# Kernel optimization log

Hardware: AMD Instinct MI355X
Metric: run time of the kernel (lower is better)

## Reference

```python
import jax, jax.numpy as jnp
import numpy as np

N_FEATURES = 256
SEQ_LEN = 128
N_HIDDEN = 30
N_LAYERS = 2
BATCH = 1024


def _lstm_layer(x, w_ih, w_hh, b_ih, b_hh):
    # x: [B, T, I]; w_ih: [4H, I]; w_hh: [4H, H]; biases: [4H]
    # PyTorch gate order: i, f, g, o
    B = x.shape[0]
    H = w_hh.shape[1]
    # precompute input contribution for all timesteps: [B, T, 4H]
    xg = jnp.einsum('bti,gi->btg', x, w_ih) + (b_ih + b_hh)
    xg = jnp.swapaxes(xg, 0, 1)  # [T, B, 4H]

    def step(carry, xg_t):
        h, c = carry
        gates = xg_t + h @ w_hh.T  # [B, 4H]
        i, f, g, o = jnp.split(gates, 4, axis=-1)
        i = jax.nn.sigmoid(i)
        f = jax.nn.sigmoid(f)
        g = jnp.tanh(g)
        o = jax.nn.sigmoid(o)
        c = f * c + i * g
        h = o * jnp.tanh(c)
        return (h, c), h

    h0 = jnp.zeros((B, H), dtype=x.dtype)
    c0 = jnp.zeros((B, H), dtype=x.dtype)
    _, hs = jax.lax.scan(step, (h0, c0), xg)
    return jnp.swapaxes(hs, 0, 1)  # [B, T, H]


def setup_inputs() -> dict:
    key = jax.random.key(0)
    ks = jax.random.split(key, 12)
    s_in = 1.0 / np.sqrt(N_HIDDEN)
    G = 4 * N_HIDDEN
    inp = {
        'x': jax.random.normal(ks[0], (BATCH, SEQ_LEN, N_FEATURES), dtype=jnp.float32),
        'w_ih0': jax.random.uniform(ks[1], (G, N_FEATURES), jnp.float32, -s_in, s_in),
        'w_hh0': jax.random.uniform(ks[2], (G, N_HIDDEN), jnp.float32, -s_in, s_in),
        'b_ih0': jax.random.uniform(ks[3], (G,), jnp.float32, -s_in, s_in),
        'b_hh0': jax.random.uniform(ks[4], (G,), jnp.float32, -s_in, s_in),
        'w_ih1': jax.random.uniform(ks[5], (G, N_HIDDEN), jnp.float32, -s_in, s_in),
        'w_hh1': jax.random.uniform(ks[6], (G, N_HIDDEN), jnp.float32, -s_in, s_in),
        'b_ih1': jax.random.uniform(ks[7], (G,), jnp.float32, -s_in, s_in),
        'b_hh1': jax.random.uniform(ks[8], (G,), jnp.float32, -s_in, s_in),
        'w_lin': jax.random.uniform(ks[9], (1, N_HIDDEN * SEQ_LEN), jnp.float32, -s_in, s_in),
        'b_lin': jax.random.uniform(ks[10], (1,), jnp.float32, -s_in, s_in),
    }
    return inp


def reference(x, w_ih0, w_hh0, b_ih0, b_hh0, w_ih1, w_hh1, b_ih1, b_hh1, w_lin, b_lin):
    h1 = _lstm_layer(x, w_ih0, w_hh0, b_ih0, b_hh0)   # [B, T, H]
    h2 = _lstm_layer(h1, w_ih1, w_hh1, b_ih1, b_hh1)  # [B, T, H]
    flat = h2.reshape(h2.shape[0], -1)                 # [B, T*H]
    return flat @ w_lin.T + b_lin                      # [B, 1]
```

## Files before the change

### kernel.cpp

```cpp
#include <hip/hip_runtime.h>

#define T_SEQ 128
#define NF 256
#define NH 30
#define NG 120
#define NBATCH 1024
#define M_ROWS (NBATCH * T_SEQ)

#define BIAS_OFF 0
#define BHI_OFF  1024
#define BLO_OFF  (BHI_OFF + 65536)
#define XG_OFF_B (BLO_OFF + 65536)

typedef __attribute__((ext_vector_type(8))) short short8;
typedef __attribute__((ext_vector_type(2))) float float2v;
typedef __attribute__((ext_vector_type(4))) float float4v;

__device__ __forceinline__ short bf16_of(float f) {
  union { float f; unsigned u; } v; v.f = f;
  unsigned r = v.u + 0x7fffu + ((v.u >> 16) & 1u);
  return (short)(r >> 16);
}
__device__ __forceinline__ float f_of_bf16(short s) {
  union { unsigned u; float f; } v; v.u = ((unsigned)(unsigned short)s) << 16;
  return v.f;
}

__device__ __forceinline__ float fast_rcp(float x) { return __builtin_amdgcn_rcpf(x); }

#define L2E 1.4426950408889634f
__device__ __forceinline__ float sigm_fast(float x) {
  float e = __builtin_amdgcn_exp2f(-L2E * x);
  return fast_rcp(1.0f + e);
}
__device__ __forceinline__ float act_a(float x, float kIn_l2, float kOut, float cOut) {
  float e = __builtin_amdgcn_exp2f(-kIn_l2 * x);
  return fmaf(kOut, fast_rcp(1.0f + e), cOut);
}
__device__ __forceinline__ float tanh_fast(float x) {
  float e = __builtin_amdgcn_exp2f(-2.0f * L2E * x);
  return fmaf(2.0f, fast_rcp(1.0f + e), -1.0f);
}

__device__ __forceinline__ float2v fma2(float2v a, float2v b, float2v c) {
  return __builtin_elementwise_fma(a, b, c);
}

__global__ void prep_kernel(const float* __restrict__ w_ih0,
                            const float* __restrict__ b_ih0,
                            const float* __restrict__ b_hh0,
                            unsigned char* __restrict__ ws) {
  int gid = blockIdx.x * 256 + threadIdx.x;
  float* bias = (float*)(ws + BIAS_OFF);
  if (gid < 128) {
    int og = (gid & 3) * NH + (gid >> 2);
    bias[gid] = (gid < NG) ? (b_ih0[og] + b_hh0[og]) : 0.0f;
  }

  int lane = gid & 63;
  int ts = gid >> 6;
  int t = ts >> 3, s = ts & 7;
  int n = s * 16 + (lane & 15);
  int orig = (n & 3) * NH + (n >> 2);
  int k0 = t * 32 + (lane >> 4) * 8;

  short8 hi, lo;
#pragma unroll
  for (int j = 0; j < 8; ++j) {
    float v = (n < NG) ? w_ih0[orig * NF + k0 + j] : 0.0f;
    short h = bf16_of(v);
    hi[j] = h;
    lo[j] = bf16_of(v - f_of_bf16(h));
  }
  *(short8*)(ws + BHI_OFF + (size_t)gid * 16) = hi;
  *(short8*)(ws + BLO_OFF + (size_t)gid * 16) = lo;
}

__global__ __launch_bounds__(256, 3) void gemm_xg(const float* __restrict__ x,
                                                  const unsigned char* __restrict__ ws,
                                                  float* __restrict__ xg) {
  __shared__ short lds_B[2][8 * 2 * 64 * 8];
  const int tid = threadIdx.x;
  const int lane = tid & 63;
  const int wave = tid >> 6;
  const int r15 = lane & 15;
  const int quad = lane >> 4;
  const int rowbase = blockIdx.x * 128 + wave * 32;

  const short* __restrict__ Bhi = (const short*)(ws + BHI_OFF);
  const short* __restrict__ Blo = (const short*)(ws + BLO_OFF);
  const float* __restrict__ bias = (const float*)(ws + BIAS_OFF);

  float4v acc[2][8];
#pragma unroll
  for (int s = 0; s < 8; ++s) {
    float b = bias[s * 16 + r15];
    float4v bv = {b, b, b, b};
    acc[0][s] = bv;
    acc[1][s] = bv;
  }

  const float* xptr[2];
  xptr[0] = x + (size_t)(rowbase + r15) * NF + quad * 8;
  xptr[1] = x + (size_t)(rowbase + 16 + r15) * NF + quad * 8;

#pragma unroll
  for (int i = 0; i < 2; ++i) {
    int s = wave * 2 + i;
    const short* ghi = Bhi + ((size_t)(0 * 8 + s) * 64 + lane) * 8;
    const short* glo = Blo + ((size_t)(0 * 8 + s) * 64 + lane) * 8;
    short* lhi = &lds_B[0][(s * 2 + 0) * 64 * 8];
    short* llo = &lds_B[0][(s * 2 + 1) * 64 * 8];
    __builtin_amdgcn_global_load_lds((const __attribute__((address_space(1))) void*)ghi,
                                     (__attribute__((address_space(3))) void*)lhi, 16, 0, 0);
    __builtin_amdgcn_global_load_lds((const __attribute__((address_space(1))) void*)glo,
                                     (__attribute__((address_space(3))) void*)llo, 16, 0, 0);
  }

  short8 ahi[2], alo[2];
#pragma unroll
  for (int g = 0; g < 2; ++g) {
    float4 p0 = *(const float4*)(xptr[g] + 0);
    float4 p1 = *(const float4*)(xptr[g] + 4);
    float f[8] = {p0.x, p0.y, p0.z, p0.w, p1.x, p1.y, p1.z, p1.w};
#pragma unroll
    for (int j = 0; j < 8; ++j) {
      short h = bf16_of(f[j]);
      ahi[g][j] = h;
      alo[g][j] = bf16_of(f[j] - f_of_bf16(h));
    }
  }
  __syncthreads();

  for (int t = 0; t < 8; ++t) {
    const int buf = t & 1;
    float4 anx[2][2];
    if (t < 7) {
#pragma unroll
      for (int i = 0; i < 2; ++i) {
        int s = wave * 2 + i;
        const short* ghi = Bhi + ((size_t)((t + 1) * 8 + s) * 64 + lane) * 8;
        const short* glo = Blo + ((size_t)((t + 1) * 8 + s) * 64 + lane) * 8;
        short* lhi = &lds_B[buf ^ 1][(s * 2 + 0) * 64 * 8];
        short* llo = &lds_B[buf ^ 1][(s * 2 + 1) * 64 * 8];
        __builtin_amdgcn_global_load_lds((const __attribute__((address_space(1))) void*)ghi,
                                         (__attribute__((address_space(3))) void*)lhi, 16, 0, 0);
        __builtin_amdgcn_global_load_lds((const __attribute__((address_space(1))) void*)glo,
                                         (__attribute__((address_space(3))) void*)llo, 16, 0, 0);
      }
#pragma unroll
      for (int g = 0; g < 2; ++g) {
        anx[g][0] = *(const float4*)(xptr[g] + (t + 1) * 32);
        anx[g][1] = *(const float4*)(xptr[g] + (t + 1) * 32 + 4);
      }
    }

#pragma unroll
    for (int s = 0; s < 8; ++s) {
      const short8 bh = *(const short8*)&lds_B[buf][((s * 2 + 0) * 64 + lane) * 8];
      const short8 bl = *(const short8*)&lds_B[buf][((s * 2 + 1) * 64 + lane) * 8];
#pragma unroll
      for (int g = 0; g < 2; ++g) {
        acc[g][s] = __builtin_amdgcn_mfma_f32_16x16x32_bf16(ahi[g], bh, acc[g][s], 0, 0, 0);
        acc[g][s] = __builtin_amdgcn_mfma_f32_16x16x32_bf16(ahi[g], bl, acc[g][s], 0, 0, 0);
        acc[g][s] = __builtin_amdgcn_mfma_f32_16x16x32_bf16(alo[g], bh, acc[g][s], 0, 0, 0);
      }
    }

    if (t < 7) {
#pragma unroll
      for (int g = 0; g < 2; ++g) {
        float f[8] = {anx[g][0].x, anx[g][0].y, anx[g][0].z, anx[g][0].w,
                      anx[g][1].x, anx[g][1].y, anx[g][1].z, anx[g][1].w};
#pragma unroll
        for (int j = 0; j < 8; ++j) {
          short h = bf16_of(f[j]);
          ahi[g][j] = h;
          alo[g][j] = bf16_of(f[j] - f_of_bf16(h));
        }
      }
    }
    __syncthreads();
  }

#pragma unroll
  for (int g = 0; g < 2; ++g) {
    const int row0 = rowbase + g * 16 + quad * 4;
#pragma unroll
    for (int s = 0; s < 8; ++s) {
      const int col = s * 16 + r15;
      if (col < NG) {
#pragma unroll
        for (int i = 0; i < 4; ++i) {
          xg[(size_t)(row0 + i) * NG + col] = acc[g][s][i];
        }
      }
    }
  }
}

__global__ __launch_bounds__(64, 1) void lstm_fused(const float* __restrict__ xg,
                                                    const float* __restrict__ w_hh0,
                                                    const float* __restrict__ w_ih1,
                                                    const float* __restrict__ w_hh1,
                                                    const float* __restrict__ b_ih1,
                                                    const float* __restrict__ b_hh1,
                                                    const float* __restrict__ w_lin,
                                                    const float* __restrict__ b_lin,
                                                    float* __restrict__ out) {
  __shared__ __align__(16) float hbuf0[32];
  __shared__ __align__(16) float hbuf1[32];
  const int b = blockIdx.x;
  const int lane = threadIdx.x;
  const bool hiHalf = lane >= 32;
  const int l = hiHalf ? (lane - 32) : lane;
  const int lc = (l < NH) ? l : (NH - 1);
  const int gA = hiHalf ? (60 + lc) : lc;
  const int gB = gA + NH;

  const float kInA = (hiHalf ? 2.0f : 1.0f) * L2E;
  const float kOutA = hiHalf ? 2.0f : 1.0f;
  const float cOutA = hiHalf ? -1.0f : 0.0f;

  float2v W0A[15], W0B[15], V1A[15], V1B[15], U1A[15], U1B[15];
#pragma unroll
  for (int p = 0; p < 15; ++p) {
    W0A[p] = *(const float2v*)&w_hh0[gA * NH + 2 * p];
    W0B[p] = *(const float2v*)&w_hh0[gB * NH + 2 * p];
    V1A[p] = *(const float2v*)&w_ih1[gA * NH + 2 * p];
    V1B[p] = *(const float2v*)&w_ih1[gB * NH + 2 * p];
    U1A[p] = *(const float2v*)&w_hh1[gA * NH + 2 * p];
    U1B[p] = *(const float2v*)&w_hh1[gB * NH + 2 * p];
  }
  const float bA1 = b_ih1[gA] + b_hh1[gA];
  const float bB1 = b_ih1[gB] + b_hh1[gB];

  float4v h0q[8], h1q[8];
#pragma unroll
  for (int k = 0; k < 8; ++k) {
    h0q[k] = float4v{0.f, 0.f, 0.f, 0.f};
    h1q[k] = float4v{0.f, 0.f, 0.f, 0.f};
  }

  float c0 = 0.0f, c1 = 0.0f, acc = 0.0f;
  const float* __restrict__ xgb = xg + (size_t)b * T_SEQ * NG;
  const int xoff = 4 * lc + (hiHalf ? 2 : 0);

  float2v xab[4];
  float wlr[4];
#pragma unroll
  for (int p = 0; p < 3; ++p) {
    xab[p] = *(const float2v*)&xgb[p * NG + xoff];
    wlr[p] = w_lin[p * NH + lc];
  }

#pragma unroll 4
  for (int t = 0; t < T_SEQ; ++t) {
    const int cur = t & 3;
    const int nxt = (t + 3) & 3;
    const int tp = (t + 3 < T_SEQ) ? (t + 3) : (T_SEQ - 1);
    float2v pxg = *(const float2v*)&xgb[tp * NG + xoff];
    float pwl = w_lin[tp * NH + lc];

    float2v a0A = {xab[cur].x, 0.f};
    float2v a0B = {xab[cur].y, 0.f};
#pragma unroll
    for (int k = 0; k < 8; ++k) {
      float2v hlo = __builtin_shufflevector(h0q[k], h0q[k], 0, 1);
      a0A = fma2(hlo, W0A[2 * k], a0A);
      a0B = fma2(hlo, W0B[2 * k], a0B);
      if (k < 7) {
        float2v hhi = __builtin_shufflevector(h0q[k], h0q[k], 2, 3);
        a0A = fma2(hhi, W0A[2 * k + 1], a0A);
        a0B = fma2(hhi, W0B[2 * k + 1], a0B);
      }
    }
    float sA = a0A.x + a0A.y;
    float sB = a0B.x + a0B.y;
    float aA = act_a(sA, kInA, kOutA, cOutA);
    float aB = sigm_fast(sB);
    float gg = __shfl_down(aA, 32);
    float oo = __shfl_down(aB, 32);
    c0 = fmaf(aB, c0, aA * gg);
    float h0 = oo * tanh_fast(c0);
    if (lane < NH) hbuf0[lane] = h0;
#pragma unroll
    for (int k = 0; k < 8; ++k) h0q[k] = *(const float4v*)&hbuf0[4 * k];

    float2v aUA = {bA1, 0.f};
    float2v aUB = {bB1, 0.f};
#pragma unroll
    for (int k = 0; k < 8; ++k) {
      float2v hlo = __builtin_shufflevector(h1q[k], h1q[k], 0, 1);
      aUA = fma2(hlo, U1A[2 * k], aUA);
      aUB = fma2(hlo, U1B[2 * k], aUB);
      if (k < 7) {
        float2v hhi = __builtin_shufflevector(h1q[k], h1q[k], 2, 3);
        aUA = fma2(hhi, U1A[2 * k + 1], aUA);
        aUB = fma2(hhi, U1B[2 * k + 1], aUB);
      }
    }

    float2v aVA = {0.f, 0.f};
    float2v aVB = {0.f, 0.f};
#pragma unroll
    for (int k = 0; k < 8; ++k) {
      float2v hlo = __builtin_shufflevector(h0q[k], h0q[k], 0, 1);
      aVA = fma2(hlo, V1A[2 * k], aVA);
      aVB = fma2(hlo, V1B[2 * k], aVB);
      if (k < 7) {
        float2v hhi = __builtin_shufflevector(h0q[k], h0q[k], 2, 3);
        aVA = fma2(hhi, V1A[2 * k + 1], aVA);
        aVB = fma2(hhi, V1B[2 * k + 1], aVB);
      }
    }
    float s1A = (aUA.x + aUA.y) + (aVA.x + aVA.y);
    float s1B = (aUB.x + aUB.y) + (aVB.x + aVB.y);
    float a1A = act_a(s1A, kInA, kOutA, cOutA);
    float a1B = sigm_fast(s1B);
    float gg1 = __shfl_down(a1A, 32);
    float oo1 = __shfl_down(a1B, 32);
    c1 = fmaf(a1B, c1, a1A * gg1);
    float h1 = oo1 * tanh_fast(c1);
    if (lane < NH) hbuf1[lane] = h1;
#pragma unroll
    for (int k = 0; k < 8; ++k) h1q[k] = *(const float4v*)&hbuf1[4 * k];

    acc = fmaf(h1, wlr[cur], acc);

    xab[nxt] = pxg;
    wlr[nxt] = pwl;
  }

  if (lane >= NH) acc = 0.0f;
#pragma unroll
  for (int off = 32; off > 0; off >>= 1) acc += __shfl_xor(acc, off);
  if (lane == 0) out[b] = acc + b_lin[0];
}

extern "C" void kernel_launch(void* const* d_in, const int* in_sizes, int n_in,
                              void* d_out, int out_size, void* d_ws, size_t ws_size,
                              hipStream_t stream) {
  (void)in_sizes; (void)n_in; (void)out_size; (void)ws_size;
  const float* x     = (const float*)d_in[0];
  const float* w_ih0 = (const float*)d_in[1];
  const float* w_hh0 = (const float*)d_in[2];
  const float* b_ih0 = (const float*)d_in[3];
  const float* b_hh0 = (const float*)d_in[4];
  const float* w_ih1 = (const float*)d_in[5];
  const float* w_hh1 = (const float*)d_in[6];
  const float* b_ih1 = (const float*)d_in[7];
  const float* b_hh1 = (const float*)d_in[8];
  const float* w_lin = (const float*)d_in[9];
  const float* b_lin = (const float*)d_in[10];
  unsigned char* ws = (unsigned char*)d_ws;
  float* out = (float*)d_out;
  float* xg = (float*)(ws + XG_OFF_B);

  prep_kernel<<<16, 256, 0, stream>>>(w_ih0, b_ih0, b_hh0, ws);
  gemm_xg<<<M_ROWS / 128, 256, 0, stream>>>(x, ws, xg);
  lstm_fused<<<NBATCH, 64, 0, stream>>>(xg, w_hh0, w_ih1, w_hh1,
                                        b_ih1, b_hh1, w_lin, b_lin, out);
}
```

Measured before the change: 302.3 us.

## Pipeline LSTM layers across two waves per batch with LDS staging

Splits the fused two-layer recurrence into a producer wave (layer 0 plus part of the layer-1 input projection) and a consumer wave (layer-1 recurrence), with four batch rows per 512-thread block. The waves hand off through double-buffered LDS and block barriers, so layer 0 of step t overlaps layer 1 of step t-1. Hidden-state broadcast now uses readlane instead of an LDS round trip. The cost is a block-wide barrier every step that couples the four batch rows in the block, plus higher register use from the scalar weight arrays.

```diff
diff --git a/kernel.cpp b/kernel.cpp
--- a/kernel.cpp
+++ b/kernel.cpp
@@ -6,6 +6,7 @@
 #define NG 120
 #define NBATCH 1024
 #define M_ROWS (NBATCH * T_SEQ)
+#define BPB 4
 
 #define BIAS_OFF 0
 #define BHI_OFF  1024
@@ -13,7 +14,6 @@
 #define XG_OFF_B (BLO_OFF + 65536)
 
 typedef __attribute__((ext_vector_type(8))) short short8;
-typedef __attribute__((ext_vector_type(2))) float float2v;
 typedef __attribute__((ext_vector_type(4))) float float4v;
 
 __device__ __forceinline__ short bf16_of(float f) {
@@ -26,6 +26,9 @@
   return v.f;
 }
 
+__device__ __forceinline__ float rl(float v, int j) {
+  return __int_as_float(__builtin_amdgcn_readlane(__float_as_int(v), j));
+}
 __device__ __forceinline__ float fast_rcp(float x) { return __builtin_amdgcn_rcpf(x); }
 
 #define L2E 1.4426950408889634f
@@ -42,9 +45,7 @@
   return fmaf(2.0f, fast_rcp(1.0f + e), -1.0f);
 }
 
-__device__ __forceinline__ float2v fma2(float2v a, float2v b, float2v c) {
-  return __builtin_elementwise_fma(a, b, c);
-}
+#define PIPE_BARRIER() asm volatile("s_waitcnt lgkmcnt(0)\n\ts_barrier" ::: "memory")
 
 __global__ void prep_kernel(const float* __restrict__ w_ih0,
                             const float* __restrict__ b_ih0,
@@ -199,7 +200,7 @@
   }
 }
 
-__global__ __launch_bounds__(64, 1) void lstm_fused(const float* __restrict__ xg,
+__global__ __launch_bounds__(512, 2) void lstm_pipe(const float* __restrict__ xg,
                                                     const float* __restrict__ w_hh0,
                                                     const float* __restrict__ w_ih1,
                                                     const float* __restrict__ w_hh1,
@@ -208,10 +209,16 @@
                                                     const float* __restrict__ w_lin,
                                                     const float* __restrict__ b_lin,
                                                     float* __restrict__ out) {
-  __shared__ __align__(16) float hbuf0[32];
-  __shared__ __align__(16) float hbuf1[32];
-  const int b = blockIdx.x;
-  const int lane = threadIdx.x;
+  __shared__ __align__(16) float stage[BPB][2][48];
+  __shared__ __align__(16) float vstage[BPB][2][128];
+
+  const int tid = threadIdx.x;
+  const int lane = tid & 63;
+  const int wave = tid >> 6;
+  const int bb = wave >> 1;
+  const bool isA = (wave & 1) == 0;
+  const int b = blockIdx.x * BPB + bb;
+
   const bool hiHalf = lane >= 32;
   const int l = hiHalf ? (lane - 32) : lane;
   const int lc = (l < NH) ? l : (NH - 1);
@@ -222,120 +229,159 @@
   const float kOutA = hiHalf ? 2.0f : 1.0f;
   const float cOutA = hiHalf ? -1.0f : 0.0f;
 
-  float2v W0A[15], W0B[15], V1A[15], V1B[15], U1A[15], U1B[15];
-#pragma unroll
-  for (int p = 0; p < 15; ++p) {
-    W0A[p] = *(const float2v*)&w_hh0[gA * NH + 2 * p];
-    W0B[p] = *(const float2v*)&w_hh0[gB * NH + 2 * p];
-    V1A[p] = *(const float2v*)&w_ih1[gA * NH + 2 * p];
-    V1B[p] = *(const float2v*)&w_ih1[gB * NH + 2 * p];
-    U1A[p] = *(const float2v*)&w_hh1[gA * NH + 2 * p];
-    U1B[p] = *(const float2v*)&w_hh1[gB * NH + 2 * p];
-  }
-  const float bA1 = b_ih1[gA] + b_hh1[gA];
-  const float bB1 = b_ih1[gB] + b_hh1[gB];
-
-  float4v h0q[8], h1q[8];
-#pragma unroll
-  for (int k = 0; k < 8; ++k) {
-    h0q[k] = float4v{0.f, 0.f, 0.f, 0.f};
-    h1q[k] = float4v{0.f, 0.f, 0.f, 0.f};
-  }
-
-  float c0 = 0.0f, c1 = 0.0f, acc = 0.0f;
-  const float* __restrict__ xgb = xg + (size_t)b * T_SEQ * NG;
-  const int xoff = 4 * lc + (hiHalf ? 2 : 0);
-
-  float2v xab[4];
-  float wlr[4];
-#pragma unroll
-  for (int p = 0; p < 3; ++p) {
-    xab[p] = *(const float2v*)&xgb[p * NG + xoff];
-    wlr[p] = w_lin[p * NH + lc];
-  }
+  if (isA) {
+    float W0A[NH], W0B[NH], V1A[16], V1B[16];
+#pragma unroll
+    for (int j = 0; j < NH; ++j) {
+      W0A[j] = w_hh0[gA * NH + j];
+      W0B[j] = w_hh0[gB * NH + j];
+    }
+#pragma unroll
+    for (int j = 0; j < 16; ++j) {
+      V1A[j] = w_ih1[gA * NH + j];
+      V1B[j] = w_ih1[gB * NH + j];
+    }
+
+    float hs[NH];
+#pragma unroll
+    for (int j = 0; j < NH; ++j) hs[j] = 0.0f;
+    float c0 = 0.0f;
+
+    const float* __restrict__ xgb = xg + (size_t)b * T_SEQ * NG;
+    const int xoff = 4 * lc + (hiHalf ? 2 : 0);
+    float2 xab[4];
+#pragma unroll
+    for (int p = 0; p < 3; ++p) xab[p] = *(const float2*)&xgb[p * NG + xoff];
 
 #pragma unroll 4
-  for (int t = 0; t < T_SEQ; ++t) {
-    const int cur = t & 3;
-    const int nxt = (t + 3) & 3;
-    const int tp = (t + 3 < T_SEQ) ? (t + 3) : (T_SEQ - 1);
-    float2v pxg = *(const float2v*)&xgb[tp * NG + xoff];
-    float pwl = w_lin[tp * NH + lc];
-
-    float2v a0A = {xab[cur].x, 0.f};
-    float2v a0B = {xab[cur].y, 0.f};
-#pragma unroll
-    for (int k = 0; k < 8; ++k) {
-      float2v hlo = __builtin_shufflevector(h0q[k], h0q[k], 0, 1);
-      a0A = fma2(hlo, W0A[2 * k], a0A);
-      a0B = fma2(hlo, W0B[2 * k], a0B);
-      if (k < 7) {
-        float2v hhi = __builtin_shufflevector(h0q[k], h0q[k], 2, 3);
-        a0A = fma2(hhi, W0A[2 * k + 1], a0A);
-        a0B = fma2(hhi, W0B[2 * k + 1], a0B);
-      }
-    }
-    float sA = a0A.x + a0A.y;
-    float sB = a0B.x + a0B.y;
-    float aA = act_a(sA, kInA, kOutA, cOutA);
-    float aB = sigm_fast(sB);
-    float gg = __shfl_down(aA, 32);
-    float oo = __shfl_down(aB, 32);
-    c0 = fmaf(aB, c0, aA * gg);
-    float h0 = oo * tanh_fast(c0);
-    if (lane < NH) hbuf0[lane] = h0;
-#pragma unroll
-    for (int k = 0; k < 8; ++k) h0q[k] = *(const float4v*)&hbuf0[4 * k];
-
-    float2v aUA = {bA1, 0.f};
-    float2v aUB = {bB1, 0.f};
-#pragma unroll
-    for (int k = 0; k < 8; ++k) {
-      float2v hlo = __builtin_shufflevector(h1q[k], h1q[k], 0, 1);
-      aUA = fma2(hlo, U1A[2 * k], aUA);
-      aUB = fma2(hlo, U1B[2 * k], aUB);
-      if (k < 7) {
-        float2v hhi = __builtin_shufflevector(h1q[k], h1q[k], 2, 3);
-        aUA = fma2(hhi, U1A[2 * k + 1], aUA);
-        aUB = fma2(hhi, U1B[2 * k + 1], aUB);
-      }
-    }
-
-    float2v aVA = {0.f, 0.f};
-    float2v aVB = {0.f, 0.f};
-#pragma unroll
-    for (int k = 0; k < 8; ++k) {
-      float2v hlo = __builtin_shufflevector(h0q[k], h0q[k], 0, 1);
-      aVA = fma2(hlo, V1A[2 * k], aVA);
-      aVB = fma2(hlo, V1B[2 * k], aVB);
-      if (k < 7) {
-        float2v hhi = __builtin_shufflevector(h0q[k], h0q[k], 2, 3);
-        aVA = fma2(hhi, V1A[2 * k + 1], aVA);
-        aVB = fma2(hhi, V1B[2 * k + 1], aVB);
-      }
-    }
-    float s1A = (aUA.x + aUA.y) + (aVA.x + aVA.y);
-    float s1B = (aUB.x + aUB.y) + (aVB.x + aVB.y);
-    float a1A = act_a(s1A, kInA, kOutA, cOutA);
-    float a1B = sigm_fast(s1B);
-    float gg1 = __shfl_down(a1A, 32);
-    float oo1 = __shfl_down(a1B, 32);
-    c1 = fmaf(a1B, c1, a1A * gg1);
-    float h1 = oo1 * tanh_fast(c1);
-    if (lane < NH) hbuf1[lane] = h1;
-#pragma unroll
-    for (int k = 0; k < 8; ++k) h1q[k] = *(const float4v*)&hbuf1[4 * k];
-
-    acc = fmaf(h1, wlr[cur], acc);
-
-    xab[nxt] = pxg;
-    wlr[nxt] = pwl;
-  }
-
-  if (lane >= NH) acc = 0.0f;
-#pragma unroll
-  for (int off = 32; off > 0; off >>= 1) acc += __shfl_xor(acc, off);
-  if (lane == 0) out[b] = acc + b_lin[0];
+    for (int s = 0; s < T_SEQ; ++s) {
+      const int cur = s & 3;
+      const int nxt = (s + 3) & 3;
+      const int tp = (s + 3 < T_SEQ) ? (s + 3) : (T_SEQ - 1);
+      float2 px = *(const float2*)&xgb[tp * NG + xoff];
+
+      float sA = xab[cur].x, sB = xab[cur].y, sA2 = 0.0f, sB2 = 0.0f;
+#pragma unroll
+      for (int j = 0; j < NH; j += 2) {
+        sA = fmaf(hs[j], W0A[j], sA);
+        sB = fmaf(hs[j], W0B[j], sB);
+        sA2 = fmaf(hs[j + 1], W0A[j + 1], sA2);
+        sB2 = fmaf(hs[j + 1], W0B[j + 1], sB2);
+      }
+      sA += sA2;
+      sB += sB2;
+      float aA = act_a(sA, kInA, kOutA, cOutA);
+      float aB = sigm_fast(sB);
+      float gg = __shfl_down(aA, 32);
+      float oo = __shfl_down(aB, 32);
+      c0 = fmaf(aB, c0, aA * gg);
+      float h0 = oo * tanh_fast(c0);
+
+#pragma unroll
+      for (int j = 0; j < NH; ++j) hs[j] = rl(h0, j);
+
+      float vA = 0.0f, vB = 0.0f, vA2 = 0.0f, vB2 = 0.0f;
+#pragma unroll
+      for (int j = 0; j < 16; j += 2) {
+        vA = fmaf(hs[j], V1A[j], vA);
+        vB = fmaf(hs[j], V1B[j], vB);
+        vA2 = fmaf(hs[j + 1], V1A[j + 1], vA2);
+        vB2 = fmaf(hs[j + 1], V1B[j + 1], vB2);
+      }
+      vA += vA2;
+      vB += vB2;
+
+      const int p = s & 1;
+      if (lane < NH) stage[bb][p][lane] = h0;
+      *(float2*)&vstage[bb][p][2 * lane] = make_float2(vA, vB);
+      xab[nxt] = px;
+
+      PIPE_BARRIER();
+    }
+    PIPE_BARRIER();
+  } else {
+    float U1A[NH], U1B[NH], V1A2[14], V1B2[14];
+#pragma unroll
+    for (int j = 0; j < NH; ++j) {
+      U1A[j] = w_hh1[gA * NH + j];
+      U1B[j] = w_hh1[gB * NH + j];
+    }
+#pragma unroll
+    for (int k = 0; k < 14; ++k) {
+      V1A2[k] = w_ih1[gA * NH + 16 + k];
+      V1B2[k] = w_ih1[gB * NH + 16 + k];
+    }
+    const float bA1 = b_ih1[gA] + b_hh1[gA];
+    const float bB1 = b_ih1[gB] + b_hh1[gB];
+
+    float h1s[NH];
+#pragma unroll
+    for (int j = 0; j < NH; ++j) h1s[j] = 0.0f;
+    float c1 = 0.0f, acc = 0.0f;
+
+    float wlr[4];
+#pragma unroll
+    for (int p = 0; p < 3; ++p) wlr[p] = w_lin[p * NH + lc];
+
+    PIPE_BARRIER();
+
+#pragma unroll 4
+    for (int t = 0; t < T_SEQ; ++t) {
+      const int cur = t & 3;
+      const int nxt = (t + 3) & 3;
+      const int tp = (t + 3 < T_SEQ) ? (t + 3) : (T_SEQ - 1);
+      float pwl = w_lin[tp * NH + lc];
+      const int p = t & 1;
+
+      float2 vp = *(const float2*)&vstage[bb][p][2 * lane];
+      float4 hA = *(const float4*)&stage[bb][p][16];
+      float4 hBv = *(const float4*)&stage[bb][p][20];
+      float4 hC = *(const float4*)&stage[bb][p][24];
+      float2 hD = *(const float2*)&stage[bb][p][28];
+
+      float suA = bA1, suB = bB1, suA2 = 0.0f, suB2 = 0.0f;
+#pragma unroll
+      for (int j = 0; j < NH; j += 2) {
+        suA = fmaf(h1s[j], U1A[j], suA);
+        suB = fmaf(h1s[j], U1B[j], suB);
+        suA2 = fmaf(h1s[j + 1], U1A[j + 1], suA2);
+        suB2 = fmaf(h1s[j + 1], U1B[j + 1], suB2);
+      }
+
+      float h0u[14] = {hA.x, hA.y, hA.z, hA.w, hBv.x, hBv.y, hBv.z, hBv.w,
+                       hC.x, hC.y, hC.z, hC.w, hD.x, hD.y};
+      float svA = vp.x, svB = vp.y, svA2 = 0.0f, svB2 = 0.0f;
+#pragma unroll
+      for (int k = 0; k < 14; k += 2) {
+        svA = fmaf(h0u[k], V1A2[k], svA);
+        svB = fmaf(h0u[k], V1B2[k], svB);
+        svA2 = fmaf(h0u[k + 1], V1A2[k + 1], svA2);
+        svB2 = fmaf(h0u[k + 1], V1B2[k + 1], svB2);
+      }
+      float s1A = (suA + suA2) + (svA + svA2);
+      float s1B = (suB + suB2) + (svB + svB2);
+
+      float a1A = act_a(s1A, kInA, kOutA, cOutA);
+      float a1B = sigm_fast(s1B);
+      float gg1 = __shfl_down(a1A, 32);
+      float oo1 = __shfl_down(a1B, 32);
+      c1 = fmaf(a1B, c1, a1A * gg1);
+      float h1 = oo1 * tanh_fast(c1);
+
+#pragma unroll
+      for (int j = 0; j < NH; ++j) h1s[j] = rl(h1, j);
+
+      acc = fmaf(h1, wlr[cur], acc);
+      wlr[nxt] = pwl;
+
+      PIPE_BARRIER();
+    }
+
+    if (lane >= NH) acc = 0.0f;
+#pragma unroll
+    for (int off = 32; off > 0; off >>= 1) acc += __shfl_xor(acc, off);
+    if (lane == 0) out[b] = acc + b_lin[0];
+  }
 }
 
 extern "C" void kernel_launch(void* const* d_in, const int* in_sizes, int n_in,
@@ -359,6 +405,6 @@
 
   prep_kernel<<<16, 256, 0, stream>>>(w_ih0, b_ih0, b_hh0, ws);
   gemm_xg<<<M_ROWS / 128, 256, 0, stream>>>(x, ws, xg);
-  lstm_fused<<<NBATCH, 64, 0, stream>>>(xg, w_hh0, w_ih1, w_hh1,
-                                        b_ih1, b_hh1, w_lin, b_lin, out);
-}
+  lstm_pipe<<<NBATCH / BPB, 512, 0, stream>>>(xg, w_hh0, w_ih1, w_hh1,
+                                              b_ih1, b_hh1, w_lin, b_lin, out);
+}
```

Measured after the change: 310.2 us. 2.6% more time.
